# Performance work log

Hardware: AMD Instinct MI355X
Metric: run time of the kernel (lower is better)

Reference implementation:

```python
import jax, jax.numpy as jnp
import numpy as np

N_NODES = 50000
N_EDGES = 800000
IN_FEATS = 128
OUT_FEATS = 128
NUM_CHANNELS = 4


def setup_inputs() -> dict:
    key = jax.random.key(0)
    ks = jax.random.split(key, 8)
    node_state = jax.random.normal(ks[0], (N_NODES, IN_FEATS), dtype=jnp.float32)
    edge_weights = jax.random.uniform(ks[1], (N_EDGES, NUM_CHANNELS), dtype=jnp.float32)
    stdv = 1.0 / np.sqrt(OUT_FEATS)
    weight = jax.random.uniform(ks[2], (IN_FEATS, OUT_FEATS, NUM_CHANNELS),
                                dtype=jnp.float32, minval=-stdv, maxval=stdv)
    stdv_b = 1.0 / np.sqrt(OUT_FEATS)
    bias = jax.random.uniform(ks[3], (OUT_FEATS, NUM_CHANNELS),
                              dtype=jnp.float32, minval=-stdv_b, maxval=stdv_b)
    lim = 1.0 / np.sqrt(OUT_FEATS)
    final_w = jax.random.uniform(ks[4], (OUT_FEATS, OUT_FEATS),
                                 dtype=jnp.float32, minval=-lim, maxval=lim)
    final_b = jax.random.uniform(ks[5], (OUT_FEATS,), dtype=jnp.float32,
                                 minval=-lim, maxval=lim)
    src = jax.random.randint(ks[6], (N_EDGES,), 0, N_NODES, dtype=jnp.int32)
    dst = jax.random.randint(ks[7], (N_EDGES,), 0, N_NODES, dtype=jnp.int32)
    return {"node_state": node_state, "edge_weights": edge_weights,
            "weight": weight, "bias": bias,
            "final_w": final_w, "final_b": final_b,
            "src": src, "dst": dst}


def reference(node_state, edge_weights, weight, bias, final_w, final_b, src, dst):
    # out_feats >= in_feats branch: aggregate raw features first, then matmul.
    N = node_state.shape[0]
    C = edge_weights.shape[1]
    x_src = node_state[src]  # [E, F] gather once (same across channels)
    h = None
    for c in range(C):  # small fixed channel count
        # edge-weighted sparse aggregation: sum_{e: dst(e)=v} w_e[c] * x[src(e)]
        agg = jax.ops.segment_sum(x_src * edge_weights[:, c:c + 1], dst,
                                  num_segments=N)  # [N, F]
        hc = jax.nn.relu(agg @ weight[:, :, c] + bias[:, c])  # [N, out]
        h = hc if h is None else h + hc  # aggr_mode='sum'
    # final nn.Linear: x @ W^T + b
    return h @ final_w.T + final_b
```

## Files before the change

kernel.cpp:

```cpp
#include <hip/hip_runtime.h>
#include <hip/hip_bf16.h>

#define N_NODES 50000
#define N_EDGES 800000
#define FEAT 128
#define CH 4
#define TM 16
#define NSCAN 49

typedef __attribute__((ext_vector_type(8))) __bf16 bf16x8;
typedef __attribute__((ext_vector_type(4))) float  f32x4;

static __device__ __forceinline__ unsigned short f2bf(float x) {
    union { float f; unsigned u; } v; v.f = x;
    unsigned r = v.u + 0x7fffu + ((v.u >> 16) & 1u);
    return (unsigned short)(r >> 16);
}
static __device__ __forceinline__ unsigned packbf2(float a, float b) {
    return (unsigned)f2bf(a) | ((unsigned)f2bf(b) << 16);
}

#define RANGE_A (N_NODES * 64)
#define RANGE_B (CH * 4 * 8 * 64)
#define RANGE_C (4 * 8 * 64)

__global__ __launch_bounds__(256) void pack_all_kernel(
        const float* __restrict__ ns, const float* __restrict__ w,
        const float* __restrict__ fw,
        unsigned* __restrict__ nsbf, uint4* __restrict__ wf,
        uint4* __restrict__ ff, int* __restrict__ deg) {
    int idx = blockIdx.x * 256 + threadIdx.x;
    if (idx < RANGE_A) {
        const float2 x = ((const float2*)ns)[idx];
        nsbf[idx] = packbf2(x.x, x.y);
        if (idx < N_NODES) deg[idx] = 0;
        return;
    }
    idx -= RANGE_A;
    if (idx < RANGE_B) {
        const int lane = idx & 63;
        const int ct   = (idx >> 6) & 7;
        const int kt   = (idx >> 9) & 3;
        const int c    = idx >> 11;
        const int o    = ct * 16 + (lane & 15);
        const int f0   = kt * 32 + (lane >> 4) * 8;
        unsigned r[4];
        #pragma unroll
        for (int p = 0; p < 4; ++p) {
            const float lo = w[((f0 + 2 * p + 0) * FEAT + o) * CH + c];
            const float hi = w[((f0 + 2 * p + 1) * FEAT + o) * CH + c];
            r[p] = packbf2(lo, hi);
        }
        wf[idx] = make_uint4(r[0], r[1], r[2], r[3]);
        return;
    }
    idx -= RANGE_B;
    if (idx < RANGE_C) {
        const int lane = idx & 63;
        const int ct   = (idx >> 6) & 7;
        const int kt   = idx >> 9;
        const int j    = ct * 16 + (lane & 15);
        const int o0   = kt * 32 + (lane >> 4) * 8;
        unsigned r[4];
        #pragma unroll
        for (int p = 0; p < 4; ++p)
            r[p] = packbf2(fw[j * FEAT + o0 + 2 * p], fw[j * FEAT + o0 + 2 * p + 1]);
        ff[idx] = make_uint4(r[0], r[1], r[2], r[3]);
    }
}

__global__ __launch_bounds__(256) void hist_kernel(const int* __restrict__ dst,
                                                   int* __restrict__ deg) {
    int e = blockIdx.x * 256 + threadIdx.x;
    if (e < N_EDGES) atomicAdd(&deg[dst[e]], 1);
}

__global__ __launch_bounds__(1024) void scanA_kernel(const int* __restrict__ deg,
                                                     int* __restrict__ offs,
                                                     int* __restrict__ bsum) {
    __shared__ int wsum[16];
    const int t = threadIdx.x, lane = t & 63, wid = t >> 6;
    const int i = blockIdx.x * 1024 + t;
    int v = (i < N_NODES) ? deg[i] : 0;
    int incl = v;
    #pragma unroll
    for (int off = 1; off < 64; off <<= 1) {
        int u = __shfl_up(incl, off, 64);
        if (lane >= off) incl += u;
    }
    if (lane == 63) wsum[wid] = incl;
    __syncthreads();
    if (t < 16) {
        int s = wsum[t];
        int sc = s;
        #pragma unroll
        for (int off = 1; off < 16; off <<= 1) {
            int u = __shfl_up(sc, off, 64);
            if (t >= off) sc += u;
        }
        wsum[t] = sc - s;
    }
    __syncthreads();
    const int excl = wsum[wid] + incl - v;
    if (i < N_NODES) offs[i] = excl;
    if (t == 1023) bsum[blockIdx.x] = excl + v;
}

__global__ __launch_bounds__(1024) void scanB_kernel(int* __restrict__ offs,
                                                     int* __restrict__ cur,
                                                     const int* __restrict__ bsum) {
    __shared__ int pfx_s;
    const int t = threadIdx.x;
    if (t < 64) {
        int v = (t < NSCAN && t < (int)blockIdx.x) ? bsum[t] : 0;
        #pragma unroll
        for (int off = 32; off > 0; off >>= 1) v += __shfl_down(v, off, 64);
        if (t == 0) pfx_s = v;
    }
    __syncthreads();
    const int pfx = pfx_s;
    const int i = blockIdx.x * 1024 + t;
    if (i < N_NODES) {
        const int v = offs[i] + pfx;
        offs[i] = v;
        cur[i] = v;
    }
    if (i == N_NODES) offs[N_NODES] = N_EDGES;
}

__global__ __launch_bounds__(256) void sortscatter_kernel(
        const int* __restrict__ src, const int* __restrict__ dst,
        int* __restrict__ cur, int2* __restrict__ sorted_se) {
    int e = blockIdx.x * 256 + threadIdx.x;
    if (e >= N_EDGES) return;
    int d = dst[e];
    int pos = atomicAdd(&cur[d], 1);
    sorted_se[pos] = make_int2(src[e], e);
}

#define EDGE_FMA(xu, ww) {                                          \
    const float xlo = __builtin_bit_cast(float, (xu) << 16);        \
    const float xhi = __builtin_bit_cast(float, (xu) & 0xffff0000u);\
    a0.x += xlo * ww.x; a0.y += xhi * ww.x;                         \
    a1.x += xlo * ww.y; a1.y += xhi * ww.y;                         \
    a2.x += xlo * ww.z; a2.y += xhi * ww.z;                         \
    a3.x += xlo * ww.w; a3.y += xhi * ww.w; }

__global__ __launch_bounds__(256) void fused_kernel(
        const unsigned* __restrict__ nsbf,
        const int* __restrict__ offs,
        const int2* __restrict__ sorted_se,
        const float4* __restrict__ ew4,
        const uint4* __restrict__ wfrag,
        const float* __restrict__ bias,
        const uint4* __restrict__ fwfrag,
        const float* __restrict__ fb,
        float* __restrict__ out) {
    __shared__ unsigned aggU[CH][TM][64];
    __shared__ unsigned short hS[TM][FEAT];
    const int t = threadIdx.x;
    const int lane = t & 63;
    const int wid = t >> 6;
    const int row0 = blockIdx.x * TM;

    for (int r = 0; r < 4; ++r) {
        const int row = wid * 4 + r;
        const int gn = row0 + row;
        float2 a0{0.f, 0.f}, a1{0.f, 0.f}, a2{0.f, 0.f}, a3{0.f, 0.f};
        {
            int e = offs[gn];
            const int end = offs[gn + 1];
            for (; e + 4 <= end; e += 4) {
                const int2 p0 = sorted_se[e + 0];
                const int2 p1 = sorted_se[e + 1];
                const int2 p2 = sorted_se[e + 2];
                const int2 p3 = sorted_se[e + 3];
                const float4 w0 = ew4[p0.y];
                const float4 w1 = ew4[p1.y];
                const float4 w2 = ew4[p2.y];
                const float4 w3 = ew4[p3.y];
                const unsigned x0 = nsbf[p0.x * 64 + lane];
                const unsigned x1 = nsbf[p1.x * 64 + lane];
                const unsigned x2 = nsbf[p2.x * 64 + lane];
                const unsigned x3 = nsbf[p3.x * 64 + lane];
                EDGE_FMA(x0, w0)
                EDGE_FMA(x1, w1)
                EDGE_FMA(x2, w2)
                EDGE_FMA(x3, w3)
            }
            for (; e < end; ++e) {
                const int2 p0 = sorted_se[e];
                const float4 w0 = ew4[p0.y];
                const unsigned x0 = nsbf[p0.x * 64 + lane];
                EDGE_FMA(x0, w0)
            }
        }
        const int sw = lane ^ ((row & 7) << 2);
        aggU[0][row][sw] = packbf2(a0.x, a0.y);
        aggU[1][row][sw] = packbf2(a1.x, a1.y);
        aggU[2][row][sw] = packbf2(a2.x, a2.y);
        aggU[3][row][sw] = packbf2(a3.x, a3.y);
    }
    __syncthreads();

    const int arow = lane & 15;
    const int kg4  = (lane >> 4) << 2;
    const int asw  = (arow & 7) << 2;
    const int ct0  = wid * 2;
    const int colA = ct0 * 16 + arow;
    const int colB = colA + 16;

    f32x4 hacc0 = {0.f, 0.f, 0.f, 0.f}, hacc1 = {0.f, 0.f, 0.f, 0.f};
    #pragma unroll
    for (int c = 0; c < CH; ++c) {
        f32x4 acc0 = {0.f, 0.f, 0.f, 0.f}, acc1 = {0.f, 0.f, 0.f, 0.f};
        #pragma unroll
        for (int kt = 0; kt < 4; ++kt) {
            const uint4 au = *(const uint4*)&aggU[c][arow][(kt * 16 + kg4) ^ asw];
            const bf16x8 a  = __builtin_bit_cast(bf16x8, au);
            const bf16x8 b0 = __builtin_bit_cast(bf16x8, wfrag[((c * 4 + kt) * 8 + ct0) * 64 + lane]);
            const bf16x8 b1 = __builtin_bit_cast(bf16x8, wfrag[((c * 4 + kt) * 8 + ct0 + 1) * 64 + lane]);
            acc0 = __builtin_amdgcn_mfma_f32_16x16x32_bf16(a, b0, acc0, 0, 0, 0);
            acc1 = __builtin_amdgcn_mfma_f32_16x16x32_bf16(a, b1, acc1, 0, 0, 0);
        }
        const float bb0 = bias[colA * CH + c];
        const float bb1 = bias[colB * CH + c];
        #pragma unroll
        for (int q = 0; q < 4; ++q) {
            hacc0[q] += fmaxf(acc0[q] + bb0, 0.f);
            hacc1[q] += fmaxf(acc1[q] + bb1, 0.f);
        }
    }

    const int rrow0 = (lane >> 4) << 2;
    #pragma unroll
    for (int q = 0; q < 4; ++q) {
        const int row = rrow0 + q;
        const int s8 = (row & 7) << 3;
        hS[row][colA ^ s8] = f2bf(hacc0[q]);
        hS[row][colB ^ s8] = f2bf(hacc1[q]);
    }
    __syncthreads();

    f32x4 o0 = {0.f, 0.f, 0.f, 0.f}, o1 = {0.f, 0.f, 0.f, 0.f};
    const int asw8 = (arow & 7) << 3;
    #pragma unroll
    for (int kt = 0; kt < 4; ++kt) {
        const uint4 hu = *(const uint4*)&hS[arow][(kt * 32 + (kg4 << 1)) ^ asw8];
        const bf16x8 a  = __builtin_bit_cast(bf16x8, hu);
        const bf16x8 b0 = __builtin_bit_cast(bf16x8, fwfrag[(kt * 8 + ct0) * 64 + lane]);
        const bf16x8 b1 = __builtin_bit_cast(bf16x8, fwfrag[(kt * 8 + ct0 + 1) * 64 + lane]);
        o0 = __builtin_amdgcn_mfma_f32_16x16x32_bf16(a, b0, o0, 0, 0, 0);
        o1 = __builtin_amdgcn_mfma_f32_16x16x32_bf16(a, b1, o1, 0, 0, 0);
    }
    const float fb0 = fb[colA];
    const float fb1 = fb[colB];
    #pragma unroll
    for (int q = 0; q < 4; ++q) {
        const int gr = row0 + rrow0 + q;
        out[gr * FEAT + colA] = o0[q] + fb0;
        out[gr * FEAT + colB] = o1[q] + fb1;
    }
}

extern "C" void kernel_launch(void* const* d_in, const int* in_sizes, int n_in,
                              void* d_out, int out_size, void* d_ws, size_t ws_size,
                              hipStream_t stream) {
    const float* node_state = (const float*)d_in[0];
    const float* edge_w     = (const float*)d_in[1];
    const float* weight     = (const float*)d_in[2];
    const float* bias       = (const float*)d_in[3];
    const float* final_w    = (const float*)d_in[4];
    const float* final_b    = (const float*)d_in[5];
    const int*   src        = (const int*)d_in[6];
    const int*   dst        = (const int*)d_in[7];
    float* out = (float*)d_out;

    char* ws = (char*)d_ws;
    int*      deg       = (int*)(ws + 0);
    int*      offs      = (int*)(ws + 200064);
    int*      cur       = (int*)(ws + 400128);
    int*      bsum      = (int*)(ws + 600192);
    int2*     sorted_se = (int2*)(ws + 600448);
    unsigned* nsbf      = (unsigned*)(ws + 7000448);
    uint4*    wfrag     = (uint4*)(ws + 19800448);
    uint4*    fwfrag    = (uint4*)(ws + 19931520);

    const int prep_total = RANGE_A + RANGE_B + RANGE_C;
    pack_all_kernel<<<(prep_total + 255) / 256, 256, 0, stream>>>(
        node_state, weight, final_w, nsbf, wfrag, fwfrag, deg);

    hist_kernel<<<(N_EDGES + 255) / 256, 256, 0, stream>>>(dst, deg);
    scanA_kernel<<<NSCAN, 1024, 0, stream>>>(deg, offs, bsum);
    scanB_kernel<<<NSCAN, 1024, 0, stream>>>(offs, cur, bsum);
    sortscatter_kernel<<<(N_EDGES + 255) / 256, 256, 0, stream>>>(
        src, dst, cur, sorted_se);

    fused_kernel<<<N_NODES / TM, 256, 0, stream>>>(
        nsbf, offs, sorted_se, (const float4*)edge_w,
        wfrag, bias, fwfrag, final_b, out);
}
```

Baseline: 281.9 us.

## Embed bf16 edge weights in sorted edge records and gather two edges per wave

The sort-scatter step now writes 16-byte records that hold the source index and the four channel weights packed as bf16, so the aggregation loop no longer makes a dependent random gather into edge_weights. It reuses the degree array, counting it down with atomicSub, in place of a separate cursor array. The aggregation loop splits each wave into two halves that handle alternate edges, with each lane loading 8 bytes of features, and combines the halves with a cross-half shuffle. The cost is a larger sorted buffer, masked tail iterations, and extra rounding from storing the weights in bf16.

```diff
diff --git a/kernel.cpp b/kernel.cpp
--- a/kernel.cpp
+++ b/kernel.cpp
@@ -18,6 +18,12 @@
 }
 static __device__ __forceinline__ unsigned packbf2(float a, float b) {
     return (unsigned)f2bf(a) | ((unsigned)f2bf(b) << 16);
+}
+static __device__ __forceinline__ float bfl(unsigned u) {
+    return __builtin_bit_cast(float, u << 16);
+}
+static __device__ __forceinline__ float bfh(unsigned u) {
+    return __builtin_bit_cast(float, u & 0xffff0000u);
 }
 
 #define RANGE_A (N_NODES * 64)
@@ -107,7 +113,6 @@
 }
 
 __global__ __launch_bounds__(1024) void scanB_kernel(int* __restrict__ offs,
-                                                     int* __restrict__ cur,
                                                      const int* __restrict__ bsum) {
     __shared__ int pfx_s;
     const int t = threadIdx.x;
@@ -120,37 +125,27 @@
     __syncthreads();
     const int pfx = pfx_s;
     const int i = blockIdx.x * 1024 + t;
-    if (i < N_NODES) {
-        const int v = offs[i] + pfx;
-        offs[i] = v;
-        cur[i] = v;
-    }
+    if (i < N_NODES) offs[i] += pfx;
     if (i == N_NODES) offs[N_NODES] = N_EDGES;
 }
 
 __global__ __launch_bounds__(256) void sortscatter_kernel(
         const int* __restrict__ src, const int* __restrict__ dst,
-        int* __restrict__ cur, int2* __restrict__ sorted_se) {
+        const float* __restrict__ ew, const int* __restrict__ offs,
+        int* __restrict__ deg, int4* __restrict__ sorted_pe) {
     int e = blockIdx.x * 256 + threadIdx.x;
     if (e >= N_EDGES) return;
-    int d = dst[e];
-    int pos = atomicAdd(&cur[d], 1);
-    sorted_se[pos] = make_int2(src[e], e);
-}
-
-#define EDGE_FMA(xu, ww) {                                          \
-    const float xlo = __builtin_bit_cast(float, (xu) << 16);        \
-    const float xhi = __builtin_bit_cast(float, (xu) & 0xffff0000u);\
-    a0.x += xlo * ww.x; a0.y += xhi * ww.x;                         \
-    a1.x += xlo * ww.y; a1.y += xhi * ww.y;                         \
-    a2.x += xlo * ww.z; a2.y += xhi * ww.z;                         \
-    a3.x += xlo * ww.w; a3.y += xhi * ww.w; }
+    const int d = dst[e];
+    const int old = atomicSub(&deg[d], 1);
+    const float4 w = ((const float4*)ew)[e];
+    sorted_pe[offs[d] + old - 1] =
+        make_int4(src[e], (int)packbf2(w.x, w.y), (int)packbf2(w.z, w.w), 0);
+}
 
 __global__ __launch_bounds__(256) void fused_kernel(
         const unsigned* __restrict__ nsbf,
         const int* __restrict__ offs,
-        const int2* __restrict__ sorted_se,
-        const float4* __restrict__ ew4,
+        const int4* __restrict__ sorted_pe,
         const uint4* __restrict__ wfrag,
         const float* __restrict__ bias,
         const uint4* __restrict__ fwfrag,
@@ -162,44 +157,49 @@
     const int lane = t & 63;
     const int wid = t >> 6;
     const int row0 = blockIdx.x * TM;
+    const int half = lane >> 5;
+    const int l31 = lane & 31;
+    const uint2* nsbf2 = (const uint2*)nsbf;
 
     for (int r = 0; r < 4; ++r) {
         const int row = wid * 4 + r;
         const int gn = row0 + row;
-        float2 a0{0.f, 0.f}, a1{0.f, 0.f}, a2{0.f, 0.f}, a3{0.f, 0.f};
-        {
-            int e = offs[gn];
-            const int end = offs[gn + 1];
-            for (; e + 4 <= end; e += 4) {
-                const int2 p0 = sorted_se[e + 0];
-                const int2 p1 = sorted_se[e + 1];
-                const int2 p2 = sorted_se[e + 2];
-                const int2 p3 = sorted_se[e + 3];
-                const float4 w0 = ew4[p0.y];
-                const float4 w1 = ew4[p1.y];
-                const float4 w2 = ew4[p2.y];
-                const float4 w3 = ew4[p3.y];
-                const unsigned x0 = nsbf[p0.x * 64 + lane];
-                const unsigned x1 = nsbf[p1.x * 64 + lane];
-                const unsigned x2 = nsbf[p2.x * 64 + lane];
-                const unsigned x3 = nsbf[p3.x * 64 + lane];
-                EDGE_FMA(x0, w0)
-                EDGE_FMA(x1, w1)
-                EDGE_FMA(x2, w2)
-                EDGE_FMA(x3, w3)
-            }
-            for (; e < end; ++e) {
-                const int2 p0 = sorted_se[e];
-                const float4 w0 = ew4[p0.y];
-                const unsigned x0 = nsbf[p0.x * 64 + lane];
-                EDGE_FMA(x0, w0)
-            }
-        }
-        const int sw = lane ^ ((row & 7) << 2);
-        aggU[0][row][sw] = packbf2(a0.x, a0.y);
-        aggU[1][row][sw] = packbf2(a1.x, a1.y);
-        aggU[2][row][sw] = packbf2(a2.x, a2.y);
-        aggU[3][row][sw] = packbf2(a3.x, a3.y);
+        f32x4 A0 = {0.f, 0.f, 0.f, 0.f}, A1 = A0, A2 = A0, A3 = A0;
+        const int beg = offs[gn];
+        const int end = offs[gn + 1];
+        for (int e = beg; e < end; e += 8) {
+#define PAIRSLOT(EO) {                                              \
+            int ee = (EO) + half;                                   \
+            const float m = (ee < end) ? 1.f : 0.f;                 \
+            ee = min(ee, end - 1);                                  \
+            const int4 pl = sorted_pe[ee];                          \
+            const uint2 xr = nsbf2[(unsigned)pl.x * 32u + l31];     \
+            const float w0 = bfl((unsigned)pl.y) * m;               \
+            const float w1 = bfh((unsigned)pl.y) * m;               \
+            const float w2 = bfl((unsigned)pl.z) * m;               \
+            const float w3 = bfh((unsigned)pl.z) * m;               \
+            const f32x4 xv = {bfl(xr.x), bfh(xr.x), bfl(xr.y), bfh(xr.y)}; \
+            A0 += xv * w0; A1 += xv * w1; A2 += xv * w2; A3 += xv * w3; }
+            PAIRSLOT(e)
+            PAIRSLOT(e + 2)
+            PAIRSLOT(e + 4)
+            PAIRSLOT(e + 6)
+#undef PAIRSLOT
+        }
+        #pragma unroll
+        for (int q = 0; q < 4; ++q) {
+            A0[q] += __shfl_xor(A0[q], 32, 64);
+            A1[q] += __shfl_xor(A1[q], 32, 64);
+            A2[q] += __shfl_xor(A2[q], 32, 64);
+            A3[q] += __shfl_xor(A3[q], 32, 64);
+        }
+        if (lane < 32) {
+            const int widx = (2 * l31) ^ ((row & 7) << 2);
+            *(uint2*)&aggU[0][row][widx] = (uint2){packbf2(A0[0], A0[1]), packbf2(A0[2], A0[3])};
+            *(uint2*)&aggU[1][row][widx] = (uint2){packbf2(A1[0], A1[1]), packbf2(A1[2], A1[3])};
+            *(uint2*)&aggU[2][row][widx] = (uint2){packbf2(A2[0], A2[1]), packbf2(A2[2], A2[3])};
+            *(uint2*)&aggU[3][row][widx] = (uint2){packbf2(A3[0], A3[1]), packbf2(A3[2], A3[3])};
+        }
     }
     __syncthreads();
 
@@ -279,12 +279,11 @@
     char* ws = (char*)d_ws;
     int*      deg       = (int*)(ws + 0);
     int*      offs      = (int*)(ws + 200064);
-    int*      cur       = (int*)(ws + 400128);
-    int*      bsum      = (int*)(ws + 600192);
-    int2*     sorted_se = (int2*)(ws + 600448);
-    unsigned* nsbf      = (unsigned*)(ws + 7000448);
-    uint4*    wfrag     = (uint4*)(ws + 19800448);
-    uint4*    fwfrag    = (uint4*)(ws + 19931520);
+    int*      bsum      = (int*)(ws + 400192);
+    int4*     sorted_pe = (int4*)(ws + 400448);
+    unsigned* nsbf      = (unsigned*)(ws + 13200448);
+    uint4*    wfrag     = (uint4*)(ws + 26000448);
+    uint4*    fwfrag    = (uint4*)(ws + 26131520);
 
     const int prep_total = RANGE_A + RANGE_B + RANGE_C;
     pack_all_kernel<<<(prep_total + 255) / 256, 256, 0, stream>>>(
@@ -292,11 +291,10 @@
 
     hist_kernel<<<(N_EDGES + 255) / 256, 256, 0, stream>>>(dst, deg);
     scanA_kernel<<<NSCAN, 1024, 0, stream>>>(deg, offs, bsum);
-    scanB_kernel<<<NSCAN, 1024, 0, stream>>>(offs, cur, bsum);
+    scanB_kernel<<<NSCAN, 1024, 0, stream>>>(offs, bsum);
     sortscatter_kernel<<<(N_EDGES + 255) / 256, 256, 0, stream>>>(
-        src, dst, cur, sorted_se);
+        src, dst, edge_w, offs, deg, sorted_pe);
 
     fused_kernel<<<N_NODES / TM, 256, 0, stream>>>(
-        nsbf, offs, sorted_se, (const float4*)edge_w,
-        wfrag, bias, fwfrag, final_b, out);
-}
+        nsbf, offs, sorted_pe, wfrag, bias, fwfrag, final_b, out);
+}
```

Result: faster. 252.1 us (-10.6%).
